# Optimization experiments

Measured on AMD Instinct MI355X. Metric: run time of the kernel, lower is better.

## Reference

```python
import jax, jax.numpy as jnp
import numpy as np

B, S, D, H, DH, FF = 4, 4096, 1024, 16, 64, 2048
EPS = 1e-6


def setup_inputs() -> dict:
    key = jax.random.key(0)
    ks = jax.random.split(key, 8)
    s = 0.02
    return {
        "x": jax.random.normal(ks[0], (B, S, D), jnp.float32),
        "scale": jnp.ones((D,), jnp.float32),
        "qw": jax.random.normal(ks[1], (DH * H, D), jnp.float32) * s,
        "qb": jnp.zeros((DH * H,), jnp.float32),
        "kw": jax.random.normal(ks[2], (DH * H, D), jnp.float32) * s,
        "kb": jnp.zeros((DH * H,), jnp.float32),
        "vw": jax.random.normal(ks[3], (DH * H, D), jnp.float32) * s,
        "vb": jnp.zeros((DH * H,), jnp.float32),
        "ow": jax.random.normal(ks[4], (D, DH * H), jnp.float32) * s,
        "ob": jnp.zeros((D,), jnp.float32),
        "f1w": jax.random.normal(ks[5], (FF, D), jnp.float32) * s,
        "f1b": jnp.zeros((FF,), jnp.float32),
        "f2w": jax.random.normal(ks[6], (D, FF), jnp.float32) * s,
        "f2b": jnp.zeros((D,), jnp.float32),
    }


def reference(x, scale, qw, qb, kw, kb, vw, vb, ow, ob, f1w, f1b, f2w, f2b):
    def rms(h):
        return h / jnp.sqrt(jnp.mean(h * h, axis=-1, keepdims=True) + EPS) * scale

    # --- attention (faithful to the module's unusual permutes) ---
    xn = rms(x)
    q = (xn @ qw.T + qb).reshape(B, S, DH, H).transpose(0, 3, 2, 1)  # [B,H,DH,S]
    k = (xn @ kw.T + kb).reshape(B, S, DH, H).transpose(0, 3, 1, 2)  # [B,H,S,DH]
    v = (xn @ vw.T + vb).reshape(B, S, DH, H).transpose(0, 3, 2, 1)  # [B,H,DH,S]
    # scores contract over the SEQUENCE axis -> [B,H,DH,DH]
    att = jax.nn.softmax(jnp.einsum('bhds,bhse->bhde', q, k) / jnp.sqrt(jnp.float32(DH)), axis=-1)
    a = jnp.einsum('bhde,bhes->bhds', att, v)  # [B,H,DH,S]
    # torch: permute(0,2,1,3).reshape(B,-1,DH*H); row-major split of (DH,H,S) -> (S, DH*H)
    a = a.transpose(0, 2, 1, 3).reshape(B, S, DH * H)
    x = a @ ow.T + ob + x

    # --- FFN with the repo's 'SwiGLU' = x*sigmoid(x) + x ---
    xn = rms(x)
    h = xn @ f1w.T + f1b
    h = h * jax.nn.sigmoid(h) + h
    x = h @ f2w.T + f2b + x
    return x
```

## Files before the change

kernel.cpp:

```cpp
#include <hip/hip_runtime.h>
#include <math.h>

typedef unsigned short u16;
typedef __attribute__((ext_vector_type(4))) unsigned short us4;
typedef __attribute__((ext_vector_type(8))) unsigned short us8;
typedef __attribute__((ext_vector_type(4))) float f4;
typedef __attribute__((ext_vector_type(8))) short bf16x8;
typedef __attribute__((ext_vector_type(4))) float f32x4;

#define S_LEN   4096
#define D_MODEL 1024
#define N_HEAD  16
#define D_HEAD  64
#define FF_DIM  2048
#define TOKENS  16384

__device__ __forceinline__ float bf2f(u16 u) {
  union { float f; unsigned u; } x; x.u = ((unsigned)u) << 16; return x.f;
}
__device__ __forceinline__ u16 f2bf(float f) {
  union { float f; unsigned u; } x; x.f = f;
  return (u16)((x.u + 0x7FFFu + ((x.u >> 16) & 1u)) >> 16);
}

__device__ __forceinline__ void gll16(const void* g, void* l) {
  __builtin_amdgcn_global_load_lds(
      (const __attribute__((address_space(1))) void*)g,
      (__attribute__((address_space(3))) void*)l, 16, 0, 0);
}

#define BARF() do { __builtin_amdgcn_s_barrier(); asm volatile("" ::: "memory"); } while (0)

__global__ void __launch_bounds__(256)
cvt6_k(const float* __restrict__ qw, const float* __restrict__ kw,
       const float* __restrict__ vw, const float* __restrict__ ow,
       const float* __restrict__ f1w, const float* __restrict__ f2w,
       u16* __restrict__ wq, u16* __restrict__ wk, u16* __restrict__ wv,
       u16* __restrict__ wo, u16* __restrict__ w1, u16* __restrict__ w2)
{
  const int id = blockIdx.x;
  const float* src; u16* dst; int base;
  if      (id < 1024) { src = qw;  dst = wq; base = 0; }
  else if (id < 2048) { src = kw;  dst = wk; base = 1024; }
  else if (id < 3072) { src = vw;  dst = wv; base = 2048; }
  else if (id < 4096) { src = ow;  dst = wo; base = 3072; }
  else if (id < 6144) { src = f1w; dst = w1; base = 4096; }
  else                { src = f2w; dst = w2; base = 6144; }
  const size_t i = ((size_t)(id - base) * 256 + threadIdx.x) * 4;
  const f4 v = *(const f4*)(src + i);
  us4 o;
  o[0] = f2bf(v[0]); o[1] = f2bf(v[1]); o[2] = f2bf(v[2]); o[3] = f2bf(v[3]);
  *(us4*)(dst + i) = o;
}

__global__ void __launch_bounds__(256)
rmsnorm_k(const float* __restrict__ in, const float* __restrict__ scale,
          u16* __restrict__ out)
{
  const int row = blockIdx.x;
  const int tid = threadIdx.x;
  const f4 v = *(const f4*)(in + (size_t)row * D_MODEL + tid * 4);
  float ss = v[0]*v[0] + v[1]*v[1] + v[2]*v[2] + v[3]*v[3];
#pragma unroll
  for (int off = 32; off > 0; off >>= 1) ss += __shfl_down(ss, off, 64);
  __shared__ float red[4];
  const int wid = tid >> 6, lane = tid & 63;
  if (lane == 0) red[wid] = ss;
  __syncthreads();
  const float tot = red[0] + red[1] + red[2] + red[3];
  const float r = rsqrtf(tot * (1.0f / 1024.0f) + 1e-6f);
  const f4 sc = *(const f4*)(scale + tid * 4);
  us4 o;
  o[0] = f2bf(v[0] * r * sc[0]);
  o[1] = f2bf(v[1] * r * sc[1]);
  o[2] = f2bf(v[2] * r * sc[2]);
  o[3] = f2bf(v[3] * r * sc[3]);
  *(us4*)(out + (size_t)row * D_MODEL + tid * 4) = o;
}

template<int EPI>
__global__ __launch_bounds__(512, 4)
void g8k(const u16* __restrict__ Ag, const u16* __restrict__ Wg,
         const float* __restrict__ bq, const float* __restrict__ bk,
         const float* __restrict__ bv, const float* __restrict__ res,
         void* __restrict__ C0, void* __restrict__ C1, void* __restrict__ C2,
         int N, int K)
{
  __shared__ __align__(16) u16 lds[36864];
  const int tid = threadIdx.x;
  const int w = tid >> 6, l = tid & 63;
  const int fr = l & 15, fq = l >> 4;
  const int wm = w >> 1, wn = w & 1;
  const int m0 = blockIdx.x << 8, n0 = blockIdx.y << 7;
  const int srow = w * 16 + (l >> 2);
  const int scol = (((l & 3) ^ ((l >> 3) & 3)) << 3);
  const int NT = K >> 5;

  auto STAGE_A = [&](int bfs, int h, int nt) {
    const int ks = (nt < NT ? nt << 5 : 0) + scol;
    gll16(Ag + (size_t)(m0 + h * 128 + srow) * K + ks,
          lds + bfs * 12288 + h * 4096 + w * 512);
  };
  auto STAGE_B = [&](int bfs, int nt) {
    const int ks = (nt < NT ? nt << 5 : 0) + scol;
    gll16(Wg + (size_t)(n0 + srow) * K + ks,
          lds + bfs * 12288 + 8192 + w * 512);
  };

  f32x4 acc[4][4] = {};
  bf16x8 afr[4], bfr[4];
  const int rsw = (fq ^ ((fr >> 1) & 3)) << 3;
  const int abase = (wm * 64 + fr) * 32 + rsw;
  const int bbase = 8192 + (wn * 64 + fr) * 32 + rsw;

  STAGE_A(0, 0, 0); STAGE_A(0, 1, 0); STAGE_B(0, 0);
  STAGE_A(1, 0, 1); STAGE_A(1, 1, 1); STAGE_B(1, 1);
  asm volatile("s_waitcnt vmcnt(3)" ::: "memory");
  BARF();

#pragma unroll 3
  for (int t = 0; t < NT; ++t) {
    const int buf = t % 3, buf2 = (t + 2) % 3;
    const int bo = buf * 12288;
#pragma unroll
    for (int mi = 0; mi < 4; ++mi)
      afr[mi] = *(const bf16x8*)(lds + bo + abase + mi * 512);
#pragma unroll
    for (int ni = 0; ni < 4; ++ni)
      bfr[ni] = *(const bf16x8*)(lds + bo + bbase + ni * 512);
    STAGE_A(buf2, 0, t + 2); STAGE_A(buf2, 1, t + 2); STAGE_B(buf2, t + 2);
    __builtin_amdgcn_s_setprio(1);
#pragma unroll
    for (int mi = 0; mi < 4; ++mi)
#pragma unroll
      for (int ni = 0; ni < 4; ++ni)
        acc[mi][ni] = __builtin_amdgcn_mfma_f32_16x16x32_bf16(afr[mi], bfr[ni],
                                                              acc[mi][ni], 0, 0, 0);
    __builtin_amdgcn_s_setprio(0);
    asm volatile("s_waitcnt vmcnt(3)" ::: "memory");
    BARF();
  }
  asm volatile("s_waitcnt vmcnt(0)" ::: "memory");
  __syncthreads();

  if constexpr (EPI == 2) {
    float* C = (float*)C0;
#pragma unroll
    for (int mi = 0; mi < 4; ++mi)
#pragma unroll
      for (int ni = 0; ni < 4; ++ni) {
        const int c = n0 + wn * 64 + ni * 16 + fr;
        const int r0 = m0 + wm * 64 + mi * 16 + fq * 4;
        const float bb = bq[c];
#pragma unroll
        for (int j = 0; j < 4; ++j)
          C[(size_t)(r0 + j) * N + c] = acc[mi][ni][j] + bb + res[(size_t)(r0 + j) * N + c];
      }
  } else if constexpr (EPI == 3) {
    u16* C = (u16*)C0;
#pragma unroll
    for (int mi = 0; mi < 4; ++mi)
#pragma unroll
      for (int ni = 0; ni < 4; ++ni) {
        const int c = n0 + wn * 64 + ni * 16 + fr;
        const int r0 = m0 + wm * 64 + mi * 16 + fq * 4;
        const float bb = bq[c];
#pragma unroll
        for (int j = 0; j < 4; ++j) {
          const float v = acc[mi][ni][j] + bb;
          const float sig = 1.0f / (1.0f + expf(-v));
          C[(size_t)(r0 + j) * N + c] = f2bf(v * sig + v);
        }
      }
  } else {
    const int z = blockIdx.y >> 3;
    const float* bias = z == 0 ? bq : (z == 1 ? bk : bv);
    const int n0l = n0 & 1023;
    const int bb = m0 >> 12, s0l = m0 & (S_LEN - 1);
#pragma unroll
    for (int mi = 0; mi < 4; ++mi)
#pragma unroll
      for (int ni = 0; ni < 4; ++ni) {
        const int c = wn * 64 + ni * 16 + fr;
        const int r0 = wm * 64 + mi * 16 + fq * 4;
        const float bv_ = bias[n0l + c];
        us4 pk;
#pragma unroll
        for (int j = 0; j < 4; ++j) pk[j] = f2bf(acc[mi][ni][j] + bv_);
        const int byte = ((c << 9) + (r0 << 1)) ^ ((c & 7) << 4);
        *(us4*)((char*)lds + byte) = pk;
      }
    __syncthreads();
    if (z < 2) {
      u16* Cout = z == 0 ? (u16*)C0 : (u16*)C1;
      const int c = tid & 127, sb = tid >> 7;
      const int o = n0l + c, d = o >> 4, h = o & 15;
      const int xr = (c & 7) << 4;
      u16* dst = Cout + ((size_t)((bb << 10) + (h << 6) + d)) * S_LEN + s0l + sb * 64;
#pragma unroll
      for (int u = 0; u < 8; ++u) {
        const int byte = ((c << 9) + (sb << 7) + (u << 4)) ^ xr;
        const us8 v = *(const us8*)((char*)lds + byte);
        *(us8*)(dst + u * 8) = v;
      }
    } else {
      u16* Cv = (u16*)C2;
      const int d0 = n0l >> 4;
#pragma unroll
      for (int q = 0; q < 8; ++q) {
        const int idx = q * 512 + tid;
        const int h = idx >> 8, s = idx & 255;
        const int xr = (h & 7) << 4;
        us8 o;
#pragma unroll
        for (int k = 0; k < 8; ++k)
          o[k] = *(const u16*)((char*)lds + ((((h + k * 16) << 9) + (s << 1)) ^ xr));
        u16* dst = Cv + ((size_t)(bb * 16 + h) * S_LEN + s0l + s) * 64 + d0;
        *(us8*)dst = o;
      }
    }
  }
}

__global__ void __launch_bounds__(256)
att_sm_k(const u16* __restrict__ qt, const u16* __restrict__ kt,
         u16* __restrict__ P)
{
  __shared__ float red[4][64][64];
  const int bh = blockIdx.x;
  const int tid = threadIdx.x, w = tid >> 6, l = tid & 63;
  const int fr = l & 15, fq = l >> 4;
  const u16* Qb = qt + (size_t)bh * D_HEAD * S_LEN;
  const u16* Kb = kt + (size_t)bh * D_HEAD * S_LEN;
  f32x4 acc[4][4] = {};
  const int sb = w * 1024 + fq * 8;
  for (int ks = 0; ks < 32; ++ks) {
    const int s0 = sb + ks * 32;
    bf16x8 a[4], b[4];
#pragma unroll
    for (int m = 0; m < 4; ++m)
      a[m] = *(const bf16x8*)(Qb + (size_t)(m*16 + fr) * S_LEN + s0);
#pragma unroll
    for (int n = 0; n < 4; ++n)
      b[n] = *(const bf16x8*)(Kb + (size_t)(n*16 + fr) * S_LEN + s0);
#pragma unroll
    for (int m = 0; m < 4; ++m)
#pragma unroll
      for (int n = 0; n < 4; ++n)
        acc[m][n] = __builtin_amdgcn_mfma_f32_16x16x32_bf16(a[m], b[n], acc[m][n], 0, 0, 0);
  }
#pragma unroll
  for (int m = 0; m < 4; ++m)
#pragma unroll
    for (int n = 0; n < 4; ++n)
      *(f32x4*)&red[w][n*16 + fr][m*16 + fq*4] = acc[m][n];
  __syncthreads();

  const int d = tid >> 2, sub = tid & 3;
  float p[16];
  float mx = -1e30f;
#pragma unroll
  for (int i = 0; i < 16; ++i) {
    const int e = sub * 16 + i;
    float v = red[0][e][d] + red[1][e][d] + red[2][e][d] + red[3][e][d];
    v *= 0.125f;
    p[i] = v; mx = fmaxf(mx, v);
  }
  mx = fmaxf(mx, __shfl_xor(mx, 1, 64));
  mx = fmaxf(mx, __shfl_xor(mx, 2, 64));
  float sm = 0.0f;
#pragma unroll
  for (int i = 0; i < 16; ++i) { p[i] = expf(p[i] - mx); sm += p[i]; }
  sm += __shfl_xor(sm, 1, 64);
  sm += __shfl_xor(sm, 2, 64);
  const float inv = 1.0f / sm;
  us8 o0, o1;
#pragma unroll
  for (int i = 0; i < 8; ++i) { o0[i] = f2bf(p[i] * inv); o1[i] = f2bf(p[i+8] * inv); }
  u16* dst = P + (size_t)bh * 4096 + d * 64 + sub * 16;
  *(us8*)dst = o0;
  *(us8*)(dst + 8) = o1;
}

__global__ void __launch_bounds__(256)
pv2_k(const u16* __restrict__ P, const u16* __restrict__ v2,
      u16* __restrict__ ar)
{
  const int bh = blockIdx.x, sc = blockIdx.y;
  const int b = bh >> 4, h = bh & 15;
  const int tid = threadIdx.x, w = tid >> 6, l = tid & 63;
  const int fr = l & 15, fq = l >> 4;
  const u16* Pb = P + (size_t)bh * 4096;
  const u16* Vb = v2 + (size_t)bh * D_HEAD * S_LEN;

  bf16x8 a[4][2];
#pragma unroll
  for (int m = 0; m < 4; ++m)
#pragma unroll
    for (int ks = 0; ks < 2; ++ks)
      a[m][ks] = *(const bf16x8*)(Pb + (m*16 + fr) * 64 + ks*32 + fq*8);

  const int sw = sc * 512 + w * 128;
  f32x4 acc[8][4] = {};
#pragma unroll
  for (int n = 0; n < 8; ++n) {
    const u16* vp = Vb + (size_t)(sw + n*16 + fr) * 64 + fq*8;
    const bf16x8 b0 = *(const bf16x8*)(vp);
    const bf16x8 b1 = *(const bf16x8*)(vp + 32);
#pragma unroll
    for (int m = 0; m < 4; ++m)
      acc[n][m] = __builtin_amdgcn_mfma_f32_16x16x32_bf16(a[m][0], b0, acc[n][m], 0, 0, 0);
#pragma unroll
    for (int m = 0; m < 4; ++m)
      acc[n][m] = __builtin_amdgcn_mfma_f32_16x16x32_bf16(a[m][1], b1, acc[n][m], 0, 0, 0);
  }

  const int shi = sc >> 1;
  const int col0 = (sc & 1) * 512 + w * 128;
#pragma unroll
  for (int m = 0; m < 4; ++m)
#pragma unroll
    for (int j = 0; j < 4; ++j) {
      const int d = m*16 + fq*4 + j;
      const size_t base = ((size_t)b * 4096 + (d << 6) + (h << 2) + shi) * 1024 + col0;
#pragma unroll
      for (int n = 0; n < 8; ++n)
        ar[base + n*16 + fr] = f2bf(acc[n][m][j]);
    }
}

extern "C" void kernel_launch(void* const* d_in, const int* in_sizes, int n_in,
                              void* d_out, int out_size, void* d_ws, size_t ws_size,
                              hipStream_t stream)
{
  const float* x     = (const float*)d_in[0];
  const float* scale = (const float*)d_in[1];
  const float* qw = (const float*)d_in[2];
  const float* qb = (const float*)d_in[3];
  const float* kw = (const float*)d_in[4];
  const float* kb = (const float*)d_in[5];
  const float* vw = (const float*)d_in[6];
  const float* vb = (const float*)d_in[7];
  const float* ow = (const float*)d_in[8];
  const float* ob = (const float*)d_in[9];
  const float* f1w = (const float*)d_in[10];
  const float* f1b = (const float*)d_in[11];
  const float* f2w = (const float*)d_in[12];
  const float* f2b = (const float*)d_in[13];
  float* out = (float*)d_out;

  const size_t TOKD = (size_t)TOKENS * D_MODEL;
  const size_t WSZ1 = (size_t)D_MODEL * D_MODEL;
  const size_t WSZ2 = (size_t)FF_DIM * D_MODEL;
  u16* xn = (u16*)d_ws;
  u16* qt = xn + TOKD;
  u16* kt = qt + TOKD;
  u16* v2 = kt + TOKD;
  u16* wq = v2 + TOKD;
  u16* wk = wq + WSZ1;
  u16* wv = wk + WSZ1;
  u16* wo = wv + WSZ1;
  u16* w1 = wo + WSZ1;
  u16* w2 = w1 + WSZ2;
  u16* Patt = w2 + WSZ2;
  u16* hbuf = kt;
  u16* ar = qt;

  dim3 blk(256);
  dim3 blk8(512);

  cvt6_k<<<8192, blk, 0, stream>>>(qw, kw, vw, ow, f1w, f2w, wq, wk, wv, wo, w1, w2);
  rmsnorm_k<<<TOKENS, blk, 0, stream>>>(x, scale, xn);
  g8k<0><<<dim3(TOKENS / 256, 24), blk8, 0, stream>>>(
      xn, wq, qb, kb, vb, nullptr, qt, kt, v2, 3072, D_MODEL);
  att_sm_k<<<64, blk, 0, stream>>>(qt, kt, Patt);
  pv2_k<<<dim3(64, 8), blk, 0, stream>>>(Patt, v2, ar);
  g8k<2><<<dim3(TOKENS / 256, D_MODEL / 128), blk8, 0, stream>>>(
      ar, wo, ob, nullptr, nullptr, x, out, nullptr, nullptr, D_MODEL, D_MODEL);
  rmsnorm_k<<<TOKENS, blk, 0, stream>>>(out, scale, xn);
  g8k<3><<<dim3(TOKENS / 256, FF_DIM / 128), blk8, 0, stream>>>(
      xn, w1, f1b, nullptr, nullptr, nullptr, hbuf, nullptr, nullptr, FF_DIM, D_MODEL);
  g8k<2><<<dim3(TOKENS / 256, D_MODEL / 128), blk8, 0, stream>>>(
      hbuf, w2, f2b, nullptr, nullptr, out, out, nullptr, nullptr, D_MODEL, FF_DIM);
}
```

Measured before the change: 495.3 us.

## Switch GEMM to 128x256 tiles with BK=64 single-buffer loop

Changes the GEMM tile from 256x128 with a 3-stage BK=32 ring buffer to a 128x256 tile with a single BK=64 LDS buffer, loaded with plain syncthreads before and after each k-step. The warp layout becomes 2x4, the swizzle is adapted to 64-wide rows, and the QKV epilogue transposes and launch grids are updated to match. This halves the number of barrier-separated k-iterations per tile. It gives up overlap between global loads and MFMA compute, so load latency is now exposed each iteration.

```diff
diff --git a/kernel.cpp b/kernel.cpp
--- a/kernel.cpp
+++ b/kernel.cpp
@@ -28,8 +28,6 @@
       (const __attribute__((address_space(1))) void*)g,
       (__attribute__((address_space(3))) void*)l, 16, 0, 0);
 }
-
-#define BARF() do { __builtin_amdgcn_s_barrier(); asm volatile("" ::: "memory"); } while (0)
 
 __global__ void __launch_bounds__(256)
 cvt6_k(const float* __restrict__ qw, const float* __restrict__ kw,
@@ -86,61 +84,50 @@
          void* __restrict__ C0, void* __restrict__ C1, void* __restrict__ C2,
          int N, int K)
 {
-  __shared__ __align__(16) u16 lds[36864];
+  __shared__ __align__(16) u16 lds[32768];
   const int tid = threadIdx.x;
   const int w = tid >> 6, l = tid & 63;
   const int fr = l & 15, fq = l >> 4;
-  const int wm = w >> 1, wn = w & 1;
-  const int m0 = blockIdx.x << 8, n0 = blockIdx.y << 7;
-  const int srow = w * 16 + (l >> 2);
-  const int scol = (((l & 3) ^ ((l >> 3) & 3)) << 3);
-  const int NT = K >> 5;
-
-  auto STAGE_A = [&](int bfs, int h, int nt) {
-    const int ks = (nt < NT ? nt << 5 : 0) + scol;
-    gll16(Ag + (size_t)(m0 + h * 128 + srow) * K + ks,
-          lds + bfs * 12288 + h * 4096 + w * 512);
-  };
-  auto STAGE_B = [&](int bfs, int nt) {
-    const int ks = (nt < NT ? nt << 5 : 0) + scol;
-    gll16(Wg + (size_t)(n0 + srow) * K + ks,
-          lds + bfs * 12288 + 8192 + w * 512);
-  };
+  const int wm = w >> 2, wn = w & 3;
+  const int m0 = blockIdx.x << 7, n0 = blockIdx.y << 8;
+  const int srow = w * 8 + (l >> 3);
+  const int scol = ((l & 7) ^ (l >> 3)) << 3;
+  const int NT = K >> 6;
 
   f32x4 acc[4][4] = {};
-  bf16x8 afr[4], bfr[4];
-  const int rsw = (fq ^ ((fr >> 1) & 3)) << 3;
-  const int abase = (wm * 64 + fr) * 32 + rsw;
-  const int bbase = 8192 + (wn * 64 + fr) * 32 + rsw;
-
-  STAGE_A(0, 0, 0); STAGE_A(0, 1, 0); STAGE_B(0, 0);
-  STAGE_A(1, 0, 1); STAGE_A(1, 1, 1); STAGE_B(1, 1);
-  asm volatile("s_waitcnt vmcnt(3)" ::: "memory");
-  BARF();
-
-#pragma unroll 3
+  const int rx = fr & 7;
+
   for (int t = 0; t < NT; ++t) {
-    const int buf = t % 3, buf2 = (t + 2) % 3;
-    const int bo = buf * 12288;
-#pragma unroll
-    for (int mi = 0; mi < 4; ++mi)
-      afr[mi] = *(const bf16x8*)(lds + bo + abase + mi * 512);
-#pragma unroll
-    for (int ni = 0; ni < 4; ++ni)
-      bfr[ni] = *(const bf16x8*)(lds + bo + bbase + ni * 512);
-    STAGE_A(buf2, 0, t + 2); STAGE_A(buf2, 1, t + 2); STAGE_B(buf2, t + 2);
-    __builtin_amdgcn_s_setprio(1);
-#pragma unroll
-    for (int mi = 0; mi < 4; ++mi)
+    const int k0 = (t << 6) + scol;
+    __syncthreads();
+    gll16(Ag + (size_t)(m0 + srow)        * K + k0, lds + w * 512);
+    gll16(Ag + (size_t)(m0 + 64 + srow)   * K + k0, lds + (8 + w) * 512);
+    gll16(Wg + (size_t)(n0 + srow)        * K + k0, lds + (16 + w) * 512);
+    gll16(Wg + (size_t)(n0 + 64 + srow)   * K + k0, lds + (24 + w) * 512);
+    gll16(Wg + (size_t)(n0 + 128 + srow)  * K + k0, lds + (32 + w) * 512);
+    gll16(Wg + (size_t)(n0 + 192 + srow)  * K + k0, lds + (40 + w) * 512);
+    __syncthreads();
+#pragma unroll
+    for (int kk = 0; kk < 2; ++kk) {
+      bf16x8 a[4], b[4];
+#pragma unroll
+      for (int mi = 0; mi < 4; ++mi)
+        a[mi] = *(const bf16x8*)(lds + (wm * 64 + mi * 16 + fr) * 64
+                                 + ((((kk << 2) + fq) ^ rx) << 3));
 #pragma unroll
       for (int ni = 0; ni < 4; ++ni)
-        acc[mi][ni] = __builtin_amdgcn_mfma_f32_16x16x32_bf16(afr[mi], bfr[ni],
-                                                              acc[mi][ni], 0, 0, 0);
-    __builtin_amdgcn_s_setprio(0);
-    asm volatile("s_waitcnt vmcnt(3)" ::: "memory");
-    BARF();
-  }
-  asm volatile("s_waitcnt vmcnt(0)" ::: "memory");
+        b[ni] = *(const bf16x8*)(lds + 8192 + (wn * 64 + ni * 16 + fr) * 64
+                                 + ((((kk << 2) + fq) ^ rx) << 3));
+      __builtin_amdgcn_s_setprio(1);
+#pragma unroll
+      for (int mi = 0; mi < 4; ++mi)
+#pragma unroll
+        for (int ni = 0; ni < 4; ++ni)
+          acc[mi][ni] = __builtin_amdgcn_mfma_f32_16x16x32_bf16(a[mi], b[ni],
+                                                                acc[mi][ni], 0, 0, 0);
+      __builtin_amdgcn_s_setprio(0);
+    }
+  }
   __syncthreads();
 
   if constexpr (EPI == 2) {
@@ -173,7 +160,7 @@
         }
       }
   } else {
-    const int z = blockIdx.y >> 3;
+    const int z = blockIdx.y >> 2;
     const float* bias = z == 0 ? bq : (z == 1 ? bk : bv);
     const int n0l = n0 & 1023;
     const int bb = m0 >> 12, s0l = m0 & (S_LEN - 1);
@@ -187,19 +174,19 @@
         us4 pk;
 #pragma unroll
         for (int j = 0; j < 4; ++j) pk[j] = f2bf(acc[mi][ni][j] + bv_);
-        const int byte = ((c << 9) + (r0 << 1)) ^ ((c & 7) << 4);
+        const int byte = ((c << 8) + (r0 << 1)) ^ ((c & 7) << 4);
         *(us4*)((char*)lds + byte) = pk;
       }
     __syncthreads();
     if (z < 2) {
       u16* Cout = z == 0 ? (u16*)C0 : (u16*)C1;
-      const int c = tid & 127, sb = tid >> 7;
+      const int c = tid & 255, half = tid >> 8;
       const int o = n0l + c, d = o >> 4, h = o & 15;
       const int xr = (c & 7) << 4;
-      u16* dst = Cout + ((size_t)((bb << 10) + (h << 6) + d)) * S_LEN + s0l + sb * 64;
+      u16* dst = Cout + ((size_t)((bb << 10) + (h << 6) + d)) * S_LEN + s0l + half * 64;
 #pragma unroll
       for (int u = 0; u < 8; ++u) {
-        const int byte = ((c << 9) + (sb << 7) + (u << 4)) ^ xr;
+        const int byte = ((c << 8) + (half << 7) + (u << 4)) ^ xr;
         const us8 v = *(const us8*)((char*)lds + byte);
         *(us8*)(dst + u * 8) = v;
       }
@@ -207,16 +194,19 @@
       u16* Cv = (u16*)C2;
       const int d0 = n0l >> 4;
 #pragma unroll
-      for (int q = 0; q < 8; ++q) {
+      for (int q = 0; q < 4; ++q) {
         const int idx = q * 512 + tid;
-        const int h = idx >> 8, s = idx & 255;
+        const int h = idx >> 7, s = idx & 127;
         const int xr = (h & 7) << 4;
-        us8 o;
-#pragma unroll
-        for (int k = 0; k < 8; ++k)
-          o[k] = *(const u16*)((char*)lds + ((((h + k * 16) << 9) + (s << 1)) ^ xr));
+        us8 lo, hi;
+#pragma unroll
+        for (int dl = 0; dl < 8; ++dl) {
+          lo[dl] = *(const u16*)((char*)lds + ((((h + dl * 16) << 8) + (s << 1)) ^ xr));
+          hi[dl] = *(const u16*)((char*)lds + ((((h + (dl + 8) * 16) << 8) + (s << 1)) ^ xr));
+        }
         u16* dst = Cv + ((size_t)(bb * 16 + h) * S_LEN + s0l + s) * 64 + d0;
-        *(us8*)dst = o;
+        *(us8*)dst = lo;
+        *(us8*)(dst + 8) = hi;
       }
     }
   }
@@ -371,15 +361,15 @@
 
   cvt6_k<<<8192, blk, 0, stream>>>(qw, kw, vw, ow, f1w, f2w, wq, wk, wv, wo, w1, w2);
   rmsnorm_k<<<TOKENS, blk, 0, stream>>>(x, scale, xn);
-  g8k<0><<<dim3(TOKENS / 256, 24), blk8, 0, stream>>>(
+  g8k<0><<<dim3(TOKENS / 128, 12), blk8, 0, stream>>>(
       xn, wq, qb, kb, vb, nullptr, qt, kt, v2, 3072, D_MODEL);
   att_sm_k<<<64, blk, 0, stream>>>(qt, kt, Patt);
   pv2_k<<<dim3(64, 8), blk, 0, stream>>>(Patt, v2, ar);
-  g8k<2><<<dim3(TOKENS / 256, D_MODEL / 128), blk8, 0, stream>>>(
+  g8k<2><<<dim3(TOKENS / 128, D_MODEL / 256), blk8, 0, stream>>>(
       ar, wo, ob, nullptr, nullptr, x, out, nullptr, nullptr, D_MODEL, D_MODEL);
   rmsnorm_k<<<TOKENS, blk, 0, stream>>>(out, scale, xn);
-  g8k<3><<<dim3(TOKENS / 256, FF_DIM / 128), blk8, 0, stream>>>(
+  g8k<3><<<dim3(TOKENS / 128, FF_DIM / 256), blk8, 0, stream>>>(
       xn, w1, f1b, nullptr, nullptr, nullptr, hbuf, nullptr, nullptr, FF_DIM, D_MODEL);
-  g8k<2><<<dim3(TOKENS / 256, D_MODEL / 128), blk8, 0, stream>>>(
+  g8k<2><<<dim3(TOKENS / 128, D_MODEL / 256), blk8, 0, stream>>>(
       hbuf, w2, f2b, nullptr, nullptr, out, out, nullptr, nullptr, D_MODEL, FF_DIM);
 }
```

Measured after the change: 454.4 us. 1.09x faster.
